# Kernel tuning notes

Hardware: AMD Instinct MI355X
Metric: run time of the kernel (lower is better)

The kernel has to match this reference:

```python
import jax, jax.numpy as jnp
import numpy as np

B, T, I, H, L = 256, 256, 256, 1024, 128


def setup_inputs() -> dict:
    key = jax.random.key(0)
    ks = jax.random.split(key, 10)
    s = 0.05
    return {
        "z": jax.random.normal(ks[0], (B, L), dtype=jnp.float32),
        "seq_len": T,
        "target": jax.random.uniform(ks[1], (B, T, I), dtype=jnp.float32),
        "W_z2h": jax.random.normal(ks[2], (H, L), dtype=jnp.float32) * s,
        "b_z2h": jnp.zeros((H,), dtype=jnp.float32),
        "W_ih": jax.random.normal(ks[3], (3 * H, I), dtype=jnp.float32) * s,
        "W_hh": jax.random.normal(ks[4], (3 * H, H), dtype=jnp.float32) * s,
        "b_ih": jnp.zeros((3 * H,), dtype=jnp.float32),
        "b_hh": jnp.zeros((3 * H,), dtype=jnp.float32),
        "W_out": jax.random.normal(ks[5], (I, H), dtype=jnp.float32) * s,
        "b_out": jnp.zeros((I,), dtype=jnp.float32),
    }


def reference(z, seq_len, target, W_z2h, b_z2h, W_ih, W_hh, b_ih, b_hh, W_out, b_out):
    # h0 = tanh(Linear(z))  -- [B, H]
    h0 = jnp.tanh(z @ W_z2h.T + b_z2h)
    # Precompute input-side gate pre-activations for all steps: [T, B, 3H]
    xg = jnp.einsum("bti,gi->tbg", target, W_ih) + b_ih

    hdim = h0.shape[-1]

    def step(h, xg_t):
        hg = h @ W_hh.T + b_hh  # [B, 3H]
        xr, xz, xn = jnp.split(xg_t, 3, axis=-1)
        hr, hz, hn = jnp.split(hg, 3, axis=-1)
        r = jax.nn.sigmoid(xr + hr)
        zg = jax.nn.sigmoid(xz + hz)
        n = jnp.tanh(xn + r * hn)
        h_new = (1.0 - zg) * n + zg * h
        y = jax.nn.sigmoid(h_new @ W_out.T + b_out)  # [B, I]
        return h_new, y

    _, ys = jax.lax.scan(step, h0, xg)  # ys: [T, B, I]
    return jnp.transpose(ys, (1, 0, 2))  # [B, T, I]
```

## Files before the change

### kernel.cpp

```cpp
#include <hip/hip_runtime.h>

#define BB 256
#define TT 256
#define II 256
#define HH 1024
#define LL 128
#define K1 1280
#define GN 3072

#define RP 52
#define GP 20
#define PP 20

typedef short s8v    __attribute__((ext_vector_type(8)));
typedef float f32x4  __attribute__((ext_vector_type(4)));
typedef float f4v    __attribute__((ext_vector_type(4)));
typedef unsigned long long u64;

__device__ __forceinline__ unsigned short f2bf(float f) {
    unsigned u = __float_as_uint(f);
    u += 0x7fffu + ((u >> 16) & 1u);
    return (unsigned short)(u >> 16);
}
__device__ __forceinline__ float bf2f(unsigned short h) {
    return __uint_as_float(((unsigned)h) << 16);
}
__device__ __forceinline__ float sigm(float x) { return 1.0f / (1.0f + __expf(-x)); }

__device__ __forceinline__ u64 hload8(const unsigned short* p) {
    return __hip_atomic_load((const u64*)p, __ATOMIC_RELAXED, __HIP_MEMORY_SCOPE_AGENT);
}
__device__ __forceinline__ s8v hload16(const unsigned short* p) {
    union { u64 q[2]; s8v v; } u;
    u.q[0] = __hip_atomic_load((const u64*)p, __ATOMIC_RELAXED, __HIP_MEMORY_SCOPE_AGENT);
    u.q[1] = __hip_atomic_load((const u64*)p + 1, __ATOMIC_RELAXED, __HIP_MEMORY_SCOPE_AGENT);
    return u.v;
}
__device__ __forceinline__ void hstore8(unsigned short* p, u64 v) {
    __hip_atomic_store((u64*)p, v, __ATOMIC_RELAXED, __HIP_MEMORY_SCOPE_AGENT);
}

__device__ __forceinline__ s8v cvt8(const float* __restrict__ p) {
    const f4v lo = *(const f4v*)p;
    const f4v hi = *(const f4v*)(p + 4);
    s8v r;
    r[0] = (short)f2bf(lo[0]); r[1] = (short)f2bf(lo[1]);
    r[2] = (short)f2bf(lo[2]); r[3] = (short)f2bf(lo[3]);
    r[4] = (short)f2bf(hi[0]); r[5] = (short)f2bf(hi[1]);
    r[6] = (short)f2bf(hi[2]); r[7] = (short)f2bf(hi[3]);
    return r;
}

__global__ void k_prep_w(const float* __restrict__ Whh, const float* __restrict__ Wih,
                         unsigned short* __restrict__ Wperm) {
    int o = blockIdx.x;
    int ntt = o / 48, q = o - ntt * 48;
    int gate = q >> 4, j = ntt * 16 + (q & 15);
    int src = gate * HH + j;
    const float* sh = Whh + (size_t)src * HH;
    const float* si = Wih + (size_t)src * II;
    unsigned short* dst = Wperm + (size_t)o * K1;
    for (int k = threadIdx.x; k < K1; k += 256)
        dst[k] = f2bf(k < HH ? sh[k] : si[k - HH]);
}

__global__ void k_prep_misc(const float* __restrict__ bih, const float* __restrict__ bhh,
                            const float* __restrict__ Wout,
                            float* __restrict__ bihp, float* __restrict__ bhhp,
                            unsigned short* __restrict__ Woutb) {
    int idx = blockIdx.x * 256 + threadIdx.x;
    if (idx < GN) {
        int ntt = idx / 48, q = idx - ntt * 48;
        int gate = q >> 4, j = ntt * 16 + (q & 15);
        int src = gate * HH + j;
        bihp[idx] = bih[src];
        bhhp[idx] = bhh[src];
    }
    for (size_t i = (size_t)blockIdx.x * 256 + threadIdx.x; i < (size_t)II * HH;
         i += (size_t)gridDim.x * 256)
        Woutb[i] = f2bf(Wout[i]);
}

__global__ void k_h0(const float* __restrict__ z, const float* __restrict__ Wz,
                     const float* __restrict__ bz, unsigned short* __restrict__ hbuf) {
    int b = blockIdx.x;
    int j0 = threadIdx.x * 4;
    const f4v* zr = (const f4v*)(z + (size_t)b * LL);
    u64 packed = 0;
#pragma unroll
    for (int jj = 0; jj < 4; ++jj) {
        int j = j0 + jj;
        const f4v* wr = (const f4v*)(Wz + (size_t)j * LL);
        float s = bz[j];
#pragma unroll
        for (int i = 0; i < LL / 4; ++i) {
            f4v a = zr[i], w = wr[i];
            s += a[0] * w[0] + a[1] * w[1] + a[2] * w[2] + a[3] * w[3];
        }
        packed |= (u64)f2bf(tanhf(s)) << (16 * jj);
    }
    hstore8(hbuf + (size_t)b * HH + j0, packed);
}

__device__ __forceinline__ void proj_tile(
    const unsigned short* __restrict__ hb, const unsigned short* __restrict__ Woutb,
    float* __restrict__ out, float (*pred)[16 * PP],
    int bo, int io, int wave, int lane, int lr, int lk, int tp, float boutv) {
    f32x4 oa = {0.f, 0.f, 0.f, 0.f};
    const unsigned short* ap = hb + (size_t)(bo * 16 + lr) * HH + (wave << 8) + lk;
    const unsigned short* wp = Woutb + (size_t)(io * 16 + lr) * HH + (wave << 8) + lk;
#pragma unroll
    for (int ks = 0; ks < 8; ++ks) {
        s8v a = hload16(ap + ks * 32);
        s8v w = *(const s8v*)(wp + ks * 32);
        oa = __builtin_amdgcn_mfma_f32_16x16x32_bf16(a, w, oa, 0, 0, 0);
    }
    if (wave >= 1) {
#pragma unroll
        for (int r = 0; r < 4; ++r)
            pred[wave - 1][(((lane >> 4) << 2) + r) * PP + lr] = oa[r];
    }
    __syncthreads();
    if (wave == 0) {
#pragma unroll
        for (int r = 0; r < 4; ++r) {
            int rw = ((lane >> 4) << 2) + r;
            int idx = rw * PP + lr;
            float v = oa[r] + pred[0][idx] + pred[1][idx] + pred[2][idx] + boutv;
            out[(size_t)(bo * 16 + rw) * (TT * II) + (size_t)tp * II + io * 16 + lr] = sigm(v);
        }
    }
}

__global__ __launch_bounds__(256, 1) void dec_main(
    const float* __restrict__ tgt,
    const unsigned short* __restrict__ Wperm,
    const float* __restrict__ bihp, const float* __restrict__ bhhp,
    unsigned short* __restrict__ hbuf,
    const unsigned short* __restrict__ Woutb,
    const float* __restrict__ bout,
    float* __restrict__ out,
    unsigned* __restrict__ barr) {
    __shared__ float red[3][64 * RP];
    __shared__ float gxn[64 * GP];
    __shared__ float pred[3][16 * PP];

    const int tid = threadIdx.x;
    const int wave = tid >> 6, lane = tid & 63;
    const int lr = lane & 15;
    const int lk = (lane >> 4) << 3;
    const int bid = blockIdx.x;
    const int m = bid >> 6, nt = bid & 63;
    const int bo = (m << 2) + (nt >> 4), io = nt & 15;

    const int eb = tid & 63;
    const int ej4 = (tid >> 6) << 2;
    const int ob = nt * 48;
    float bir[4], biz[4], bixn[4], bihn[4];
#pragma unroll
    for (int jj = 0; jj < 4; ++jj) {
        int j = ej4 + jj;
        bir[jj]  = bihp[ob + j] + bhhp[ob + j];
        biz[jj]  = bihp[ob + 16 + j] + bhhp[ob + 16 + j];
        bixn[jj] = bihp[ob + 32 + j];
        bihn[jj] = bhhp[ob + 32 + j];
    }
    const float boutv = bout[io * 16 + lr];

    unsigned* mybarr = barr + m * TT;

    for (int t = 0; t < TT; ++t) {
        const unsigned short* hcur = hbuf + (size_t)(t % 3) * (BB * HH);
        unsigned short* hnxt = hbuf + (size_t)((t + 1) % 3) * (BB * HH);

        f32x4 acc[12];
#pragma unroll
        for (int i = 0; i < 12; ++i) acc[i] = (f32x4){0.f, 0.f, 0.f, 0.f};

        if (wave < 3) {
            const int kb = wave * 320;
            const unsigned short* hp0 = hcur + (size_t)(m * 64 + lr) * HH + kb + lk;
            const unsigned short* wp0 = Wperm + (size_t)(nt * 48 + lr) * K1 + kb + lk;
#pragma unroll
            for (int ks = 0; ks < 10; ++ks) {
                s8v a[4], w[3];
#pragma unroll
                for (int mi = 0; mi < 4; ++mi)
                    a[mi] = hload16(hp0 + (size_t)mi * 16 * HH + ks * 32);
#pragma unroll
                for (int ni = 0; ni < 3; ++ni)
                    w[ni] = *(const s8v*)(wp0 + (size_t)ni * 16 * K1 + ks * 32);
#pragma unroll
                for (int mi = 0; mi < 4; ++mi)
#pragma unroll
                    for (int ni = 0; ni < 3; ++ni)
                        acc[mi * 3 + ni] = __builtin_amdgcn_mfma_f32_16x16x32_bf16(
                            a[mi], w[ni], acc[mi * 3 + ni], 0, 0, 0);
            }
        } else {
            f32x4 accx[4];
#pragma unroll
            for (int i = 0; i < 4; ++i) accx[i] = (f32x4){0.f, 0.f, 0.f, 0.f};
            {
                const unsigned short* hp0 = hcur + (size_t)(m * 64 + lr) * HH + 960 + lk;
                const unsigned short* wp0 = Wperm + (size_t)(nt * 48 + lr) * K1 + 960 + lk;
#pragma unroll
                for (int ks = 0; ks < 2; ++ks) {
                    s8v a[4], w[3];
#pragma unroll
                    for (int mi = 0; mi < 4; ++mi)
                        a[mi] = hload16(hp0 + (size_t)mi * 16 * HH + ks * 32);
#pragma unroll
                    for (int ni = 0; ni < 3; ++ni)
                        w[ni] = *(const s8v*)(wp0 + (size_t)ni * 16 * K1 + ks * 32);
#pragma unroll
                    for (int mi = 0; mi < 4; ++mi)
#pragma unroll
                        for (int ni = 0; ni < 3; ++ni)
                            acc[mi * 3 + ni] = __builtin_amdgcn_mfma_f32_16x16x32_bf16(
                                a[mi], w[ni], acc[mi * 3 + ni], 0, 0, 0);
                }
            }
            {
                const float* xp0 = tgt + ((size_t)(m * 64 + lr) * TT + t) * II + lk;
                const unsigned short* wp0 = Wperm + (size_t)(nt * 48 + lr) * K1 + HH + lk;
#pragma unroll
                for (int ks = 0; ks < 8; ++ks) {
                    s8v a[4], w[3];
#pragma unroll
                    for (int mi = 0; mi < 4; ++mi)
                        a[mi] = cvt8(xp0 + (size_t)mi * 16 * TT * II + ks * 32);
#pragma unroll
                    for (int ni = 0; ni < 3; ++ni)
                        w[ni] = *(const s8v*)(wp0 + (size_t)ni * 16 * K1 + ks * 32);
#pragma unroll
                    for (int mi = 0; mi < 4; ++mi) {
                        acc[mi * 3 + 0] = __builtin_amdgcn_mfma_f32_16x16x32_bf16(a[mi], w[0], acc[mi * 3 + 0], 0, 0, 0);
                        acc[mi * 3 + 1] = __builtin_amdgcn_mfma_f32_16x16x32_bf16(a[mi], w[1], acc[mi * 3 + 1], 0, 0, 0);
                        accx[mi]        = __builtin_amdgcn_mfma_f32_16x16x32_bf16(a[mi], w[2], accx[mi], 0, 0, 0);
                    }
                }
            }
#pragma unroll
            for (int mi = 0; mi < 4; ++mi)
#pragma unroll
                for (int r = 0; r < 4; ++r)
                    gxn[(mi * 16 + ((lane >> 4) << 2) + r) * GP + lr] = accx[mi][r];
        }

        if (wave >= 1) {
            float* s = &red[wave - 1][0];
#pragma unroll
            for (int mi = 0; mi < 4; ++mi)
#pragma unroll
                for (int ni = 0; ni < 3; ++ni)
#pragma unroll
                    for (int r = 0; r < 4; ++r)
                        s[(mi * 16 + ((lane >> 4) << 2) + r) * RP + ni * 16 + lr] =
                            acc[mi * 3 + ni][r];
        }
        __syncthreads();
        if (wave == 0) {
#pragma unroll
            for (int mi = 0; mi < 4; ++mi)
#pragma unroll
                for (int ni = 0; ni < 3; ++ni)
#pragma unroll
                    for (int r = 0; r < 4; ++r) {
                        int idx = (mi * 16 + ((lane >> 4) << 2) + r) * RP + ni * 16 + lr;
                        red[0][idx] = acc[mi * 3 + ni][r] + red[0][idx] + red[1][idx] + red[2][idx];
                    }
        }
        __syncthreads();

        {
            const int bg = m * 64 + eb;
            const int jbase = nt * 16 + ej4;
            u64 hold8 = hload8(hcur + (size_t)bg * HH + jbase);
            u64 packed = 0;
#pragma unroll
            for (int jj = 0; jj < 4; ++jj) {
                int c = ej4 + jj;
                float ghr = red[0][eb * RP + c];
                float ghz = red[0][eb * RP + 16 + c];
                float ghn = red[0][eb * RP + 32 + c];
                float gx  = gxn[eb * GP + c];
                float r   = sigm(ghr + bir[jj]);
                float zg  = sigm(ghz + biz[jj]);
                float n   = tanhf(gx + bixn[jj] + r * (ghn + bihn[jj]));
                float hold = bf2f((unsigned short)(hold8 >> (16 * jj)));
                float hnew = (1.f - zg) * n + zg * hold;
                packed |= (u64)f2bf(hnew) << (16 * jj);
            }
            hstore8(hnxt + (size_t)bg * HH + jbase, packed);
        }

        asm volatile("s_waitcnt vmcnt(0)" ::: "memory");
        __syncthreads();
        if (tid == 0)
            __hip_atomic_fetch_add(mybarr + t, 1u, __ATOMIC_RELAXED, __HIP_MEMORY_SCOPE_AGENT);

        if (t > 0)
            proj_tile(hcur, Woutb, out, pred, bo, io, wave, lane, lr, lk, t - 1, boutv);

        if (tid == 0) {
            int guard = 0;
            while (__hip_atomic_load(mybarr + t, __ATOMIC_RELAXED,
                                     __HIP_MEMORY_SCOPE_AGENT) < 64u) {
                __builtin_amdgcn_s_sleep(1);
                if (++guard > (1 << 17)) break;
            }
        }
        __syncthreads();
    }
    proj_tile(hbuf + (size_t)(TT % 3) * (BB * HH), Woutb, out, pred,
              bo, io, wave, lane, lr, lk, TT - 1, boutv);
}

extern "C" void kernel_launch(void* const* d_in, const int* in_sizes, int n_in,
                              void* d_out, int out_size, void* d_ws, size_t ws_size,
                              hipStream_t stream) {
    const float* z    = (const float*)d_in[0];
    const float* tgt  = (const float*)d_in[2];
    const float* Wz2h = (const float*)d_in[3];
    const float* bz2h = (const float*)d_in[4];
    const float* Wih  = (const float*)d_in[5];
    const float* Whh  = (const float*)d_in[6];
    const float* bih  = (const float*)d_in[7];
    const float* bhh  = (const float*)d_in[8];
    const float* Wout = (const float*)d_in[9];
    const float* bout = (const float*)d_in[10];
    float* out = (float*)d_out;

    char* ws = (char*)d_ws;
    unsigned short* Wperm = (unsigned short*)ws;
    float* bihp           = (float*)(ws + 7864320);
    float* bhhp           = (float*)(ws + 7876608);
    unsigned short* Woutb = (unsigned short*)(ws + 7888896);
    unsigned short* hbuf  = (unsigned short*)(ws + 8413184);
    unsigned* barr        = (unsigned*)(ws + 9986048);

    hipMemsetAsync(barr, 0, 4 * TT * sizeof(unsigned), stream);
    hipLaunchKernelGGL(k_prep_w, dim3(GN), dim3(256), 0, stream, Whh, Wih, Wperm);
    hipLaunchKernelGGL(k_prep_misc, dim3(1024), dim3(256), 0, stream, bih, bhh, Wout,
                       bihp, bhhp, Woutb);
    hipLaunchKernelGGL(k_h0, dim3(BB), dim3(256), 0, stream, z, Wz2h, bz2h, hbuf);
    hipLaunchKernelGGL(dec_main, dim3(256), dim3(256), 0, stream,
                       tgt, Wperm, bihp, bhhp, hbuf, Woutb, bout, out, barr);
}
```

Baseline: 5.286 ms.

## Split GRU recurrence across 512 blocks with register-resident weights and per-tile flags

Doubles the persistent grid to 512 blocks (two per CU), each handling 32 batch rows, and keeps the block's W_hh/W_ih slice in registers across all timesteps instead of reloading it every step. The all-to-all counter barrier is replaced by per-tile progress flags polled with a wave ballot. The input projection is issued before the wait so it overlaps. When the workspace is large enough, a separate h buffer is kept for every timestep so plain non-atomic loads can be used. This adds heavy register pressure with 30 vector weight fragments per thread at occupancy 2, and depends on co-residency of all 512 blocks to avoid deadlock.

```diff
diff --git a/kernel.cpp b/kernel.cpp
--- a/kernel.cpp
+++ b/kernel.cpp
@@ -26,19 +26,6 @@
     return __uint_as_float(((unsigned)h) << 16);
 }
 __device__ __forceinline__ float sigm(float x) { return 1.0f / (1.0f + __expf(-x)); }
-
-__device__ __forceinline__ u64 hload8(const unsigned short* p) {
-    return __hip_atomic_load((const u64*)p, __ATOMIC_RELAXED, __HIP_MEMORY_SCOPE_AGENT);
-}
-__device__ __forceinline__ s8v hload16(const unsigned short* p) {
-    union { u64 q[2]; s8v v; } u;
-    u.q[0] = __hip_atomic_load((const u64*)p, __ATOMIC_RELAXED, __HIP_MEMORY_SCOPE_AGENT);
-    u.q[1] = __hip_atomic_load((const u64*)p + 1, __ATOMIC_RELAXED, __HIP_MEMORY_SCOPE_AGENT);
-    return u.v;
-}
-__device__ __forceinline__ void hstore8(unsigned short* p, u64 v) {
-    __hip_atomic_store((u64*)p, v, __ATOMIC_RELAXED, __HIP_MEMORY_SCOPE_AGENT);
-}
 
 __device__ __forceinline__ s8v cvt8(const float* __restrict__ p) {
     const f4v lo = *(const f4v*)p;
@@ -49,6 +36,24 @@
     r[4] = (short)f2bf(hi[0]); r[5] = (short)f2bf(hi[1]);
     r[6] = (short)f2bf(hi[2]); r[7] = (short)f2bf(hi[3]);
     return r;
+}
+
+__device__ __forceinline__ s8v hload16a(const unsigned short* p) {
+    union { u64 q[2]; s8v v; } u;
+    u.q[0] = __hip_atomic_load((const u64*)p, __ATOMIC_RELAXED, __HIP_MEMORY_SCOPE_AGENT);
+    u.q[1] = __hip_atomic_load((const u64*)p + 1, __ATOMIC_RELAXED, __HIP_MEMORY_SCOPE_AGENT);
+    return u.v;
+}
+template<int FRESH> __device__ __forceinline__ s8v ld16h(const unsigned short* p) {
+    if constexpr (FRESH) return *(const s8v*)p;
+    else return hload16a(p);
+}
+template<int FRESH> __device__ __forceinline__ unsigned ld4h(const unsigned short* p) {
+    if constexpr (FRESH) return *(const unsigned*)p;
+    else return __hip_atomic_load((const unsigned*)p, __ATOMIC_RELAXED, __HIP_MEMORY_SCOPE_AGENT);
+}
+__device__ __forceinline__ void st4h(unsigned short* p, unsigned v) {
+    __hip_atomic_store((unsigned*)p, v, __ATOMIC_RELAXED, __HIP_MEMORY_SCOPE_AGENT);
 }
 
 __global__ void k_prep_w(const float* __restrict__ Whh, const float* __restrict__ Wih,
@@ -99,19 +104,20 @@
         }
         packed |= (u64)f2bf(tanhf(s)) << (16 * jj);
     }
-    hstore8(hbuf + (size_t)b * HH + j0, packed);
-}
-
+    *(u64*)(hbuf + (size_t)b * HH + j0) = packed;
+}
+
+template<int FRESH>
 __device__ __forceinline__ void proj_tile(
-    const unsigned short* __restrict__ hb, const unsigned short* __restrict__ Woutb,
+    const unsigned short* hb, const unsigned short* __restrict__ Woutb,
     float* __restrict__ out, float (*pred)[16 * PP],
-    int bo, int io, int wave, int lane, int lr, int lk, int tp, float boutv) {
+    int brow, int io, int wave, int lane, int lr, int lk, int tp, float boutv) {
     f32x4 oa = {0.f, 0.f, 0.f, 0.f};
-    const unsigned short* ap = hb + (size_t)(bo * 16 + lr) * HH + (wave << 8) + lk;
+    const unsigned short* ap = hb + (size_t)(brow + lr) * HH + (wave << 8) + lk;
     const unsigned short* wp = Woutb + (size_t)(io * 16 + lr) * HH + (wave << 8) + lk;
 #pragma unroll
     for (int ks = 0; ks < 8; ++ks) {
-        s8v a = hload16(ap + ks * 32);
+        s8v a = ld16h<FRESH>(ap + ks * 32);
         s8v w = *(const s8v*)(wp + ks * 32);
         oa = __builtin_amdgcn_mfma_f32_16x16x32_bf16(a, w, oa, 0, 0, 0);
     }
@@ -127,122 +133,155 @@
             int rw = ((lane >> 4) << 2) + r;
             int idx = rw * PP + lr;
             float v = oa[r] + pred[0][idx] + pred[1][idx] + pred[2][idx] + boutv;
-            out[(size_t)(bo * 16 + rw) * (TT * II) + (size_t)tp * II + io * 16 + lr] = sigm(v);
-        }
-    }
-}
-
-__global__ __launch_bounds__(256, 1) void dec_main(
-    const float* __restrict__ tgt,
-    const unsigned short* __restrict__ Wperm,
-    const float* __restrict__ bihp, const float* __restrict__ bhhp,
-    unsigned short* __restrict__ hbuf,
-    const unsigned short* __restrict__ Woutb,
-    const float* __restrict__ bout,
-    float* __restrict__ out,
-    unsigned* __restrict__ barr) {
-    __shared__ float red[3][64 * RP];
-    __shared__ float gxn[64 * GP];
-    __shared__ float pred[3][16 * PP];
-
+            out[(size_t)(brow + rw) * (TT * II) + (size_t)tp * II + io * 16 + lr] = sigm(v);
+        }
+    }
+}
+
+template<int FRESH>
+__device__ void run(const float* __restrict__ tgt, const unsigned short* __restrict__ Wperm,
+                    const float* __restrict__ bihp, const float* __restrict__ bhhp,
+                    unsigned short* hbuf, const unsigned short* __restrict__ Woutb,
+                    const float* __restrict__ bout, float* __restrict__ out,
+                    unsigned* flags,
+                    float (*red)[32 * RP], float* gxn, float (*pred)[16 * PP]) {
     const int tid = threadIdx.x;
     const int wave = tid >> 6, lane = tid & 63;
     const int lr = lane & 15;
     const int lk = (lane >> 4) << 3;
     const int bid = blockIdx.x;
-    const int m = bid >> 6, nt = bid & 63;
-    const int bo = (m << 2) + (nt >> 4), io = nt & 15;
-
-    const int eb = tid & 63;
-    const int ej4 = (tid >> 6) << 2;
+    const int m = bid & 7, nt = bid >> 3;
+    const int doproj = (nt < 32);
+    const int brow = m * 32 + ((nt >> 4) & 1) * 16;
+    const int io = nt & 15;
+    const float boutv = bout[io * 16 + lr];
+
+    const int eb = tid & 31, j2 = (tid >> 5) << 1;
     const int ob = nt * 48;
-    float bir[4], biz[4], bixn[4], bihn[4];
-#pragma unroll
-    for (int jj = 0; jj < 4; ++jj) {
-        int j = ej4 + jj;
+    float bir[2], biz[2], bixn[2], bihn[2];
+#pragma unroll
+    for (int jj = 0; jj < 2; ++jj) {
+        int j = j2 + jj;
         bir[jj]  = bihp[ob + j] + bhhp[ob + j];
         biz[jj]  = bihp[ob + 16 + j] + bhhp[ob + 16 + j];
         bixn[jj] = bihp[ob + 32 + j];
         bihn[jj] = bhhp[ob + 32 + j];
     }
-    const float boutv = bout[io * 16 + lr];
-
-    unsigned* mybarr = barr + m * TT;
+
+    s8v wreg[30];
+    if (wave == 3) {
+#pragma unroll
+        for (int ks = 0; ks < 2; ++ks)
+#pragma unroll
+            for (int ni = 0; ni < 3; ++ni)
+                wreg[ks * 3 + ni] = *(const s8v*)(Wperm +
+                    (size_t)(nt * 48 + ni * 16 + lr) * K1 + 960 + ks * 32 + lk);
+#pragma unroll
+        for (int ks = 0; ks < 8; ++ks)
+#pragma unroll
+            for (int ni = 0; ni < 3; ++ni)
+                wreg[6 + ks * 3 + ni] = *(const s8v*)(Wperm +
+                    (size_t)(nt * 48 + ni * 16 + lr) * K1 + HH + ks * 32 + lk);
+    } else {
+#pragma unroll
+        for (int ks = 0; ks < 10; ++ks)
+#pragma unroll
+            for (int ni = 0; ni < 3; ++ni)
+                wreg[ks * 3 + ni] = *(const s8v*)(Wperm +
+                    (size_t)(nt * 48 + ni * 16 + lr) * K1 + wave * 320 + ks * 32 + lk);
+    }
+
+    unsigned* gflags = flags + (m << 6);
 
     for (int t = 0; t < TT; ++t) {
-        const unsigned short* hcur = hbuf + (size_t)(t % 3) * (BB * HH);
-        unsigned short* hnxt = hbuf + (size_t)((t + 1) % 3) * (BB * HH);
-
-        f32x4 acc[12];
-#pragma unroll
-        for (int i = 0; i < 12; ++i) acc[i] = (f32x4){0.f, 0.f, 0.f, 0.f};
-
-        if (wave < 3) {
-            const int kb = wave * 320;
-            const unsigned short* hp0 = hcur + (size_t)(m * 64 + lr) * HH + kb + lk;
-            const unsigned short* wp0 = Wperm + (size_t)(nt * 48 + lr) * K1 + kb + lk;
-#pragma unroll
-            for (int ks = 0; ks < 10; ++ks) {
-                s8v a[4], w[3];
-#pragma unroll
-                for (int mi = 0; mi < 4; ++mi)
-                    a[mi] = hload16(hp0 + (size_t)mi * 16 * HH + ks * 32);
-#pragma unroll
-                for (int ni = 0; ni < 3; ++ni)
-                    w[ni] = *(const s8v*)(wp0 + (size_t)ni * 16 * K1 + ks * 32);
-#pragma unroll
-                for (int mi = 0; mi < 4; ++mi)
-#pragma unroll
-                    for (int ni = 0; ni < 3; ++ni)
-                        acc[mi * 3 + ni] = __builtin_amdgcn_mfma_f32_16x16x32_bf16(
-                            a[mi], w[ni], acc[mi * 3 + ni], 0, 0, 0);
-            }
-        } else {
-            f32x4 accx[4];
-#pragma unroll
-            for (int i = 0; i < 4; ++i) accx[i] = (f32x4){0.f, 0.f, 0.f, 0.f};
-            {
-                const unsigned short* hp0 = hcur + (size_t)(m * 64 + lr) * HH + 960 + lk;
-                const unsigned short* wp0 = Wperm + (size_t)(nt * 48 + lr) * K1 + 960 + lk;
-#pragma unroll
-                for (int ks = 0; ks < 2; ++ks) {
-                    s8v a[4], w[3];
-#pragma unroll
-                    for (int mi = 0; mi < 4; ++mi)
-                        a[mi] = hload16(hp0 + (size_t)mi * 16 * HH + ks * 32);
-#pragma unroll
-                    for (int ni = 0; ni < 3; ++ni)
-                        w[ni] = *(const s8v*)(wp0 + (size_t)ni * 16 * K1 + ks * 32);
-#pragma unroll
-                    for (int mi = 0; mi < 4; ++mi)
-#pragma unroll
-                        for (int ni = 0; ni < 3; ++ni)
-                            acc[mi * 3 + ni] = __builtin_amdgcn_mfma_f32_16x16x32_bf16(
-                                a[mi], w[ni], acc[mi * 3 + ni], 0, 0, 0);
+        const unsigned short* hcur = hbuf + (size_t)(FRESH ? t : (t % 3)) * (BB * HH);
+        unsigned short* hnxt = hbuf + (size_t)(FRESH ? (t + 1) : ((t + 1) % 3)) * (BB * HH);
+
+        f32x4 acc[6];
+#pragma unroll
+        for (int i = 0; i < 6; ++i) acc[i] = (f32x4){0.f, 0.f, 0.f, 0.f};
+        f32x4 accx[2];
+        accx[0] = (f32x4){0.f, 0.f, 0.f, 0.f};
+        accx[1] = (f32x4){0.f, 0.f, 0.f, 0.f};
+
+        if (wave == 3) {
+#pragma unroll
+            for (int cx = 0; cx < 4; ++cx) {
+                s8v xa[2][2];
+#pragma unroll
+                for (int i2 = 0; i2 < 2; ++i2) {
+                    int ks = cx * 2 + i2;
+#pragma unroll
+                    for (int mi = 0; mi < 2; ++mi)
+                        xa[i2][mi] = cvt8(tgt +
+                            ((size_t)(m * 32 + mi * 16 + lr) * TT + t) * II + ks * 32 + lk);
                 }
-            }
-            {
-                const float* xp0 = tgt + ((size_t)(m * 64 + lr) * TT + t) * II + lk;
-                const unsigned short* wp0 = Wperm + (size_t)(nt * 48 + lr) * K1 + HH + lk;
-#pragma unroll
-                for (int ks = 0; ks < 8; ++ks) {
-                    s8v a[4], w[3];
-#pragma unroll
-                    for (int mi = 0; mi < 4; ++mi)
-                        a[mi] = cvt8(xp0 + (size_t)mi * 16 * TT * II + ks * 32);
-#pragma unroll
-                    for (int ni = 0; ni < 3; ++ni)
-                        w[ni] = *(const s8v*)(wp0 + (size_t)ni * 16 * K1 + ks * 32);
-#pragma unroll
-                    for (int mi = 0; mi < 4; ++mi) {
-                        acc[mi * 3 + 0] = __builtin_amdgcn_mfma_f32_16x16x32_bf16(a[mi], w[0], acc[mi * 3 + 0], 0, 0, 0);
-                        acc[mi * 3 + 1] = __builtin_amdgcn_mfma_f32_16x16x32_bf16(a[mi], w[1], acc[mi * 3 + 1], 0, 0, 0);
-                        accx[mi]        = __builtin_amdgcn_mfma_f32_16x16x32_bf16(a[mi], w[2], accx[mi], 0, 0, 0);
+#pragma unroll
+                for (int i2 = 0; i2 < 2; ++i2) {
+                    int ks = cx * 2 + i2;
+#pragma unroll
+                    for (int mi = 0; mi < 2; ++mi) {
+                        acc[mi * 3 + 0] = __builtin_amdgcn_mfma_f32_16x16x32_bf16(
+                            xa[i2][mi], wreg[6 + ks * 3 + 0], acc[mi * 3 + 0], 0, 0, 0);
+                        acc[mi * 3 + 1] = __builtin_amdgcn_mfma_f32_16x16x32_bf16(
+                            xa[i2][mi], wreg[6 + ks * 3 + 1], acc[mi * 3 + 1], 0, 0, 0);
+                        accx[mi] = __builtin_amdgcn_mfma_f32_16x16x32_bf16(
+                            xa[i2][mi], wreg[6 + ks * 3 + 2], accx[mi], 0, 0, 0);
                     }
                 }
             }
-#pragma unroll
-            for (int mi = 0; mi < 4; ++mi)
+        }
+
+        if (t > 0 && wave == 0) {
+            int guard = 0;
+            for (;;) {
+                unsigned v = __hip_atomic_load(gflags + lane, __ATOMIC_RELAXED,
+                                               __HIP_MEMORY_SCOPE_AGENT);
+                if (__ballot(v >= (unsigned)t) == ~0ull) break;
+                __builtin_amdgcn_s_sleep(1);
+                if (++guard > (1 << 18)) break;
+            }
+            asm volatile("" ::: "memory");
+        }
+        __syncthreads();
+
+        if (wave < 3) {
+#pragma unroll
+            for (int c = 0; c < 2; ++c) {
+                s8v a[5][2];
+#pragma unroll
+                for (int i = 0; i < 5; ++i)
+#pragma unroll
+                    for (int mi = 0; mi < 2; ++mi)
+                        a[i][mi] = ld16h<FRESH>(hcur +
+                            (size_t)(m * 32 + mi * 16 + lr) * HH + wave * 320 + (c * 5 + i) * 32 + lk);
+#pragma unroll
+                for (int i = 0; i < 5; ++i)
+#pragma unroll
+                    for (int mi = 0; mi < 2; ++mi)
+#pragma unroll
+                        for (int ni = 0; ni < 3; ++ni)
+                            acc[mi * 3 + ni] = __builtin_amdgcn_mfma_f32_16x16x32_bf16(
+                                a[i][mi], wreg[(c * 5 + i) * 3 + ni], acc[mi * 3 + ni], 0, 0, 0);
+            }
+        } else {
+            s8v a[2][2];
+#pragma unroll
+            for (int ks = 0; ks < 2; ++ks)
+#pragma unroll
+                for (int mi = 0; mi < 2; ++mi)
+                    a[ks][mi] = ld16h<FRESH>(hcur +
+                        (size_t)(m * 32 + mi * 16 + lr) * HH + 960 + ks * 32 + lk);
+#pragma unroll
+            for (int ks = 0; ks < 2; ++ks)
+#pragma unroll
+                for (int mi = 0; mi < 2; ++mi)
+#pragma unroll
+                    for (int ni = 0; ni < 3; ++ni)
+                        acc[mi * 3 + ni] = __builtin_amdgcn_mfma_f32_16x16x32_bf16(
+                            a[ks][mi], wreg[ks * 3 + ni], acc[mi * 3 + ni], 0, 0, 0);
+#pragma unroll
+            for (int mi = 0; mi < 2; ++mi)
 #pragma unroll
                 for (int r = 0; r < 4; ++r)
                     gxn[(mi * 16 + ((lane >> 4) << 2) + r) * GP + lr] = accx[mi][r];
@@ -251,7 +290,7 @@
         if (wave >= 1) {
             float* s = &red[wave - 1][0];
 #pragma unroll
-            for (int mi = 0; mi < 4; ++mi)
+            for (int mi = 0; mi < 2; ++mi)
 #pragma unroll
                 for (int ni = 0; ni < 3; ++ni)
 #pragma unroll
@@ -262,7 +301,7 @@
         __syncthreads();
         if (wave == 0) {
 #pragma unroll
-            for (int mi = 0; mi < 4; ++mi)
+            for (int mi = 0; mi < 2; ++mi)
 #pragma unroll
                 for (int ni = 0; ni < 3; ++ni)
 #pragma unroll
@@ -274,13 +313,13 @@
         __syncthreads();
 
         {
-            const int bg = m * 64 + eb;
-            const int jbase = nt * 16 + ej4;
-            u64 hold8 = hload8(hcur + (size_t)bg * HH + jbase);
-            u64 packed = 0;
-#pragma unroll
-            for (int jj = 0; jj < 4; ++jj) {
-                int c = ej4 + jj;
+            const int bg = m * 32 + eb;
+            const int jg = nt * 16 + j2;
+            unsigned hold = ld4h<FRESH>(hcur + (size_t)bg * HH + jg);
+            unsigned packed = 0;
+#pragma unroll
+            for (int jj = 0; jj < 2; ++jj) {
+                int c = j2 + jj;
                 float ghr = red[0][eb * RP + c];
                 float ghz = red[0][eb * RP + 16 + c];
                 float ghn = red[0][eb * RP + 32 + c];
@@ -288,33 +327,53 @@
                 float r   = sigm(ghr + bir[jj]);
                 float zg  = sigm(ghz + biz[jj]);
                 float n   = tanhf(gx + bixn[jj] + r * (ghn + bihn[jj]));
-                float hold = bf2f((unsigned short)(hold8 >> (16 * jj)));
-                float hnew = (1.f - zg) * n + zg * hold;
-                packed |= (u64)f2bf(hnew) << (16 * jj);
+                float ho  = bf2f((unsigned short)(hold >> (16 * jj)));
+                packed |= (unsigned)f2bf((1.f - zg) * n + zg * ho) << (16 * jj);
             }
-            hstore8(hnxt + (size_t)bg * HH + jbase, packed);
+            st4h(hnxt + (size_t)bg * HH + jg, packed);
         }
 
         asm volatile("s_waitcnt vmcnt(0)" ::: "memory");
         __syncthreads();
         if (tid == 0)
-            __hip_atomic_fetch_add(mybarr + t, 1u, __ATOMIC_RELAXED, __HIP_MEMORY_SCOPE_AGENT);
-
-        if (t > 0)
-            proj_tile(hcur, Woutb, out, pred, bo, io, wave, lane, lr, lk, t - 1, boutv);
-
-        if (tid == 0) {
+            __hip_atomic_store(gflags + nt, (unsigned)(t + 1), __ATOMIC_RELAXED,
+                               __HIP_MEMORY_SCOPE_AGENT);
+
+        if (doproj && t > 0)
+            proj_tile<FRESH>(hcur, Woutb, out, pred, brow, io, wave, lane, lr, lk, t - 1, boutv);
+    }
+
+    if (doproj) {
+        if (wave == 0) {
             int guard = 0;
-            while (__hip_atomic_load(mybarr + t, __ATOMIC_RELAXED,
-                                     __HIP_MEMORY_SCOPE_AGENT) < 64u) {
+            for (;;) {
+                unsigned v = __hip_atomic_load(gflags + lane, __ATOMIC_RELAXED,
+                                               __HIP_MEMORY_SCOPE_AGENT);
+                if (__ballot(v >= (unsigned)TT) == ~0ull) break;
                 __builtin_amdgcn_s_sleep(1);
-                if (++guard > (1 << 17)) break;
+                if (++guard > (1 << 18)) break;
             }
+            asm volatile("" ::: "memory");
         }
         __syncthreads();
-    }
-    proj_tile(hbuf + (size_t)(TT % 3) * (BB * HH), Woutb, out, pred,
-              bo, io, wave, lane, lr, lk, TT - 1, boutv);
+        proj_tile<FRESH>(hbuf + (size_t)(FRESH ? TT : (TT % 3)) * (BB * HH),
+                         Woutb, out, pred, brow, io, wave, lane, lr, lk, TT - 1, boutv);
+    }
+}
+
+__global__ __launch_bounds__(256, 2) void dec_main(
+    const float* __restrict__ tgt, const unsigned short* __restrict__ Wperm,
+    const float* __restrict__ bihp, const float* __restrict__ bhhp,
+    unsigned short* hbuf, const unsigned short* __restrict__ Woutb,
+    const float* __restrict__ bout, float* __restrict__ out,
+    unsigned* flags, int fresh) {
+    __shared__ float red[3][32 * RP];
+    __shared__ float gxn[32 * GP];
+    __shared__ float pred[3][16 * PP];
+    if (fresh)
+        run<1>(tgt, Wperm, bihp, bhhp, hbuf, Woutb, bout, out, flags, red, gxn, pred);
+    else
+        run<0>(tgt, Wperm, bihp, bhhp, hbuf, Woutb, bout, out, flags, red, gxn, pred);
 }
 
 extern "C" void kernel_launch(void* const* d_in, const int* in_sizes, int n_in,
@@ -337,14 +396,17 @@
     float* bihp           = (float*)(ws + 7864320);
     float* bhhp           = (float*)(ws + 7876608);
     unsigned short* Woutb = (unsigned short*)(ws + 7888896);
-    unsigned short* hbuf  = (unsigned short*)(ws + 8413184);
-    unsigned* barr        = (unsigned*)(ws + 9986048);
-
-    hipMemsetAsync(barr, 0, 4 * TT * sizeof(unsigned), stream);
+    unsigned* flags       = (unsigned*)(ws + 8413184);
+    unsigned short* hbuf  = (unsigned short*)(ws + 8415232);
+
+    const size_t need_big = 8415232ull + 257ull * 524288ull;
+    const int fresh = (ws_size >= need_big) ? 1 : 0;
+
+    hipMemsetAsync((void*)flags, 0, 2048, stream);
     hipLaunchKernelGGL(k_prep_w, dim3(GN), dim3(256), 0, stream, Whh, Wih, Wperm);
     hipLaunchKernelGGL(k_prep_misc, dim3(1024), dim3(256), 0, stream, bih, bhh, Wout,
                        bihp, bhhp, Woutb);
     hipLaunchKernelGGL(k_h0, dim3(BB), dim3(256), 0, stream, z, Wz2h, bz2h, hbuf);
-    hipLaunchKernelGGL(dec_main, dim3(256), dim3(256), 0, stream,
-                       tgt, Wperm, bihp, bhhp, hbuf, Woutb, bout, out, barr);
-}
+    hipLaunchKernelGGL(dec_main, dim3(512), dim3(256), 0, stream,
+                       tgt, Wperm, bihp, bhhp, hbuf, Woutb, bout, out, flags, fresh);
+}
```

New measurement: 5.168 ms. -2.2%, faster.
